# Performance work log

Measured on AMD Instinct MI355X. Metric: run time of the kernel, lower is better.

## Reference

```python
import jax, jax.numpy as jnp
import numpy as np
from jax import lax

NSAMPLE = 1024
SEM_NUM = 20


def weighted_fps(xyz, w, nsample):
    # xyz: [B,N,3], w: [B,N] -> idx [B,nsample] int32
    # Iterative weighted furthest point sampling: start at index 0, keep the
    # min squared distance to the selected set, pick argmax(min_dist * weight).
    B, N, _ = xyz.shape
    barange = jnp.arange(B)

    def step(carry, _):
        min_d, last = carry                      # [B,N], [B]
        lp = xyz[barange, last]                  # [B,3] last selected points
        d = jnp.sum((xyz - lp[:, None, :]) ** 2, axis=-1)  # [B,N]
        min_d = jnp.minimum(min_d, d)
        nxt = jnp.argmax(min_d * w, axis=1).astype(jnp.int32)
        return (min_d, nxt), nxt

    init = (jnp.full((B, N), 1e10, xyz.dtype), jnp.zeros((B,), jnp.int32))
    _, rest = lax.scan(step, init, None, length=nsample - 1)   # [nsample-1, B]
    idx = jnp.concatenate([jnp.zeros((1, B), jnp.int32), rest], axis=0)
    return idx.T                                               # [B, nsample]


def setup_inputs() -> dict:
    key = jax.random.key(0)
    k1, k2, k3 = jax.random.split(key, 3)
    B, N, C = 16, 16384, 128
    xyz = jax.random.normal(k1, (B, N, 3), dtype=jnp.float32)
    seg_feature = jax.random.normal(k2, (B, C, N), dtype=jnp.float32)
    seg_label = jax.random.randint(k3, (B, N), 0, SEM_NUM, dtype=jnp.int32)
    return {"xyz": xyz, "seg_feature": seg_feature, "seg_label": seg_label}


def reference(xyz, seg_feature, seg_label):
    # class frequency weights: count[b,c] = #points of class c in cloud b
    counts = jnp.sum(jax.nn.one_hot(seg_label, SEM_NUM, dtype=jnp.float32), axis=1)  # [B,SEM]
    seg_weights = jnp.take_along_axis(counts, seg_label, axis=1)                     # [B,N]
    idx = weighted_fps(lax.stop_gradient(xyz), seg_weights, NSAMPLE)                 # [B,S]
    sampled_xyz = jnp.take_along_axis(xyz, idx[:, :, None], axis=1)                  # [B,S,3]
    sample_seg_feature = jnp.take_along_axis(seg_feature, idx[:, None, :], axis=2)   # [B,C,S]
    sample_seg_label = jnp.take_along_axis(seg_label, idx, axis=1)                   # [B,S]
    return sampled_xyz, sample_seg_feature, sample_seg_label
```

## Files before the change

kernel.cpp:

```cpp
#include <hip/hip_runtime.h>


#define FPS_B   16
#define FPS_N   16384
#define FPS_C   128
#define FPS_S   1024
#define FPS_SEM 20
#define FPS_T   1024
#define FPS_PPT 16

__global__ __launch_bounds__(FPS_T)
__attribute__((amdgpu_waves_per_eu(4, 4)))
void wfps_kernel(
    const float* __restrict__ xyz,
    const int*   __restrict__ label,
    int*         __restrict__ idx_out)
{
  const int b = blockIdx.x;
  const int t = threadIdx.x;

  __shared__ int counts[FPS_SEM];
  __shared__ unsigned long long wmax[FPS_S];

  if (t < FPS_SEM) counts[t] = 0;
  wmax[t] = 0ull;
  __syncthreads();

  const int* lab = label + (long long)b * FPS_N;
  int mylab[FPS_PPT];
#pragma unroll
  for (int k = 0; k < FPS_PPT; ++k) {
    mylab[k] = lab[t + k * FPS_T];
    atomicAdd(&counts[mylab[k]], 1);
  }
  __syncthreads();

  const float* xb = xyz + (long long)b * FPS_N * 3;
  float px[FPS_PPT], py[FPS_PPT], pz[FPS_PPT], w[FPS_PPT], mind[FPS_PPT];
#pragma unroll
  for (int k = 0; k < FPS_PPT; ++k) {
    int n = t + k * FPS_T;
    px[k] = xb[n * 3 + 0];
    py[k] = xb[n * 3 + 1];
    pz[k] = xb[n * 3 + 2];
    w[k] = (float)counts[mylab[k]];
    mind[k] = 1e10f;
    asm("" : "+v"(px[k]), "+v"(py[k]), "+v"(pz[k]), "+v"(w[k]));
  }

  if (t == 0) idx_out[(long long)b * FPS_S] = 0;
  float lx = xb[0], ly = xb[1], lz = xb[2];

  for (int s = 1; s < FPS_S; ++s) {
    float bs = -1.0f;
    int bk = 0;
#pragma unroll
    for (int k = 0; k < FPS_PPT; ++k) {
      float dx = __fsub_rn(px[k], lx);
      float dy = __fsub_rn(py[k], ly);
      float dz = __fsub_rn(pz[k], lz);
      float d  = __fadd_rn(__fadd_rn(__fmul_rn(dx, dx), __fmul_rn(dy, dy)),
                           __fmul_rn(dz, dz));
      float m = fminf(mind[k], d);
      mind[k] = m;
      float sc = __fmul_rn(m, w[k]);
      bool g = sc > bs;
      bs = g ? sc : bs;
      bk = g ? k : bk;
    }
    unsigned n = (unsigned)t + ((unsigned)bk << 10);
    unsigned long long best =
        ((unsigned long long)__float_as_uint(bs) << 32) |
        (unsigned long long)(~n);

#pragma unroll
    for (int off = 32; off > 0; off >>= 1) {
      unsigned long long o = __shfl_xor(best, off, 64);
      best = (o > best) ? o : best;
    }
    if ((t & 63) == 0) atomicMax(&wmax[s], best);
    __syncthreads();
    best = wmax[s];

    int cur = (int)(~(unsigned)best);
    cur = __builtin_amdgcn_readfirstlane(cur);

    if (t == 0) idx_out[(long long)b * FPS_S + s] = cur;

    const float* q = xb + 3 * cur;
    lx = q[0]; ly = q[1]; lz = q[2];
  }
}

__global__ void gather_kernel(
    const float* __restrict__ xyz,
    const float* __restrict__ feat,
    const int*   __restrict__ label,
    const int*   __restrict__ idx,
    float*       __restrict__ out)
{
  const long long FEAT = (long long)FPS_B * FPS_C * FPS_S;
  const int XYZN = FPS_B * FPS_S * 3;
  const int LABN = FPS_B * FPS_S;
  long long i = (long long)blockIdx.x * blockDim.x + threadIdx.x;

  if (i < FEAT) {
    int s = (int)(i & (FPS_S - 1));
    int c = (int)((i >> 10) & (FPS_C - 1));
    int b = (int)(i >> 17);
    int n = idx[b * FPS_S + s];
    out[XYZN + i] = feat[((long long)(b * FPS_C + c)) * FPS_N + n];
  } else if (i < FEAT + XYZN) {
    int j = (int)(i - FEAT);
    int d = j % 3;
    int sb = j / 3;
    int s = sb & (FPS_S - 1);
    int b = sb >> 10;
    int n = idx[b * FPS_S + s];
    out[j] = xyz[((long long)b * FPS_N + n) * 3 + d];
  } else if (i < FEAT + XYZN + LABN) {
    int j = (int)(i - FEAT - XYZN);
    int s = j & (FPS_S - 1);
    int b = j >> 10;
    int n = idx[b * FPS_S + s];
    out[FEAT + XYZN + j] = (float)label[b * FPS_N + n];
  }
}

extern "C" void kernel_launch(void* const* d_in, const int* in_sizes, int n_in,
                              void* d_out, int out_size, void* d_ws, size_t ws_size,
                              hipStream_t stream) {
  const float* xyz   = (const float*)d_in[0];
  const float* feat  = (const float*)d_in[1];
  const int*   label = (const int*)d_in[2];
  float* out = (float*)d_out;
  int*   idx = (int*)d_ws;

  wfps_kernel<<<FPS_B, FPS_T, 0, stream>>>(xyz, label, idx);

  const long long total = (long long)FPS_B * FPS_C * FPS_S
                        + (long long)FPS_B * FPS_S * 3
                        + (long long)FPS_B * FPS_S;
  gather_kernel<<<(int)((total + 255) / 256), 256, 0, stream>>>(
      xyz, feat, label, idx, out);
}
```

Baseline: 1.892 ms.

## Split each batch's FPS across four workgroups with global-memory argmax exchange

Each point cloud's weighted FPS is spread over four workgroups instead of one, so 64 CUs work instead of 16 and each thread holds 4 points rather than 16. Every iteration, each workgroup publishes its local best to a per-step slot in global memory and spins until the other three slots are filled, then takes the max. A zeroing kernel clears the slots beforehand, and the old single-block kernel remains as a fallback when the workspace is too small. This relies on all 64 blocks being resident at once and adds a cross-CU round trip through global memory on every step.

```diff
diff --git a/kernel.cpp b/kernel.cpp
--- a/kernel.cpp
+++ b/kernel.cpp
@@ -6,56 +6,63 @@
 #define FPS_C   128
 #define FPS_S   1024
 #define FPS_SEM 20
-#define FPS_T   1024
-#define FPS_PPT 16
-
-__global__ __launch_bounds__(FPS_T)
-__attribute__((amdgpu_waves_per_eu(4, 4)))
-void wfps_kernel(
+#define FPS_QB  4
+#define FPS_MT  1024
+#define FPS_MP  4
+
+typedef unsigned long long ull;
+
+__global__ void zero_slots(ull* part) {
+  int i = blockIdx.x * blockDim.x + threadIdx.x;
+  part[i] = 0ull;
+}
+
+__global__ __launch_bounds__(FPS_MT) void wfps_multi(
     const float* __restrict__ xyz,
     const int*   __restrict__ label,
-    int*         __restrict__ idx_out)
+    int*         __restrict__ idx_out,
+    ull*         __restrict__ part)
 {
-  const int b = blockIdx.x;
+  const int b = blockIdx.x & 15;
+  const int q = blockIdx.x >> 4;
   const int t = threadIdx.x;
 
   __shared__ int counts[FPS_SEM];
-  __shared__ unsigned long long wmax[FPS_S];
+  __shared__ ull wmax[FPS_S];
 
   if (t < FPS_SEM) counts[t] = 0;
   wmax[t] = 0ull;
   __syncthreads();
 
-  const int* lab = label + (long long)b * FPS_N;
-  int mylab[FPS_PPT];
-#pragma unroll
-  for (int k = 0; k < FPS_PPT; ++k) {
-    mylab[k] = lab[t + k * FPS_T];
-    atomicAdd(&counts[mylab[k]], 1);
-  }
-  __syncthreads();
-
-  const float* xb = xyz + (long long)b * FPS_N * 3;
-  float px[FPS_PPT], py[FPS_PPT], pz[FPS_PPT], w[FPS_PPT], mind[FPS_PPT];
-#pragma unroll
-  for (int k = 0; k < FPS_PPT; ++k) {
-    int n = t + k * FPS_T;
+  const int* lab = label + b * FPS_N;
+#pragma unroll
+  for (int j = 0; j < 16; ++j)
+    atomicAdd(&counts[lab[t + j * FPS_MT]], 1);
+  __syncthreads();
+
+  const float* xb = xyz + b * FPS_N * 3;
+  float px[FPS_MP], py[FPS_MP], pz[FPS_MP], w[FPS_MP], mind[FPS_MP];
+#pragma unroll
+  for (int k = 0; k < FPS_MP; ++k) {
+    int n = q * 4096 + k * 1024 + t;
     px[k] = xb[n * 3 + 0];
     py[k] = xb[n * 3 + 1];
     pz[k] = xb[n * 3 + 2];
-    w[k] = (float)counts[mylab[k]];
+    w[k] = (float)counts[lab[n]];
     mind[k] = 1e10f;
     asm("" : "+v"(px[k]), "+v"(py[k]), "+v"(pz[k]), "+v"(w[k]));
   }
 
-  if (t == 0) idx_out[(long long)b * FPS_S] = 0;
+  if (q == 0 && t == 0) idx_out[b * FPS_S] = 0;
   float lx = xb[0], ly = xb[1], lz = xb[2];
+
+  ull* pb = part + b * (FPS_QB * FPS_S);
 
   for (int s = 1; s < FPS_S; ++s) {
     float bs = -1.0f;
     int bk = 0;
 #pragma unroll
-    for (int k = 0; k < FPS_PPT; ++k) {
+    for (int k = 0; k < FPS_MP; ++k) {
       float dx = __fsub_rn(px[k], lx);
       float dy = __fsub_rn(py[k], ly);
       float dz = __fsub_rn(pz[k], lz);
@@ -68,14 +75,114 @@
       bs = g ? sc : bs;
       bk = g ? k : bk;
     }
+    unsigned n = (unsigned)t + ((unsigned)bk << 10) + ((unsigned)q << 12);
+    ull best = ((ull)__float_as_uint(bs) << 32) | (ull)(~n);
+
+#pragma unroll
+    for (int off = 32; off > 0; off >>= 1) {
+      ull o = __shfl_xor(best, off, 64);
+      best = (o > best) ? o : best;
+    }
+    if ((t & 63) == 0) atomicMax(&wmax[s], best);
+    __syncthreads();
+
+    if (t == 0) {
+      ull loc = wmax[s];
+      __hip_atomic_store(&pb[q * FPS_S + s], loc,
+                         __ATOMIC_RELAXED, __HIP_MEMORY_SCOPE_AGENT);
+      const int q1 = (q + 1) & 3, q2 = (q + 2) & 3, q3 = (q + 3) & 3;
+      ull v1, v2, v3;
+      do {
+        v1 = __hip_atomic_load(&pb[q1 * FPS_S + s],
+                               __ATOMIC_RELAXED, __HIP_MEMORY_SCOPE_AGENT);
+        v2 = __hip_atomic_load(&pb[q2 * FPS_S + s],
+                               __ATOMIC_RELAXED, __HIP_MEMORY_SCOPE_AGENT);
+        v3 = __hip_atomic_load(&pb[q3 * FPS_S + s],
+                               __ATOMIC_RELAXED, __HIP_MEMORY_SCOPE_AGENT);
+      } while (!(v1 && v2 && v3));
+      ull m = loc;
+      m = (v1 > m) ? v1 : m;
+      m = (v2 > m) ? v2 : m;
+      m = (v3 > m) ? v3 : m;
+      wmax[s] = m;
+    }
+    __syncthreads();
+
+    ull g = wmax[s];
+    int cur = (int)(~(unsigned)g);
+    cur = __builtin_amdgcn_readfirstlane(cur);
+
+    if (q == 0 && t == 0) idx_out[b * FPS_S + s] = cur;
+
+    const float* qq = xb + 3 * cur;
+    lx = qq[0]; ly = qq[1]; lz = qq[2];
+  }
+}
+
+__global__ __launch_bounds__(1024)
+__attribute__((amdgpu_waves_per_eu(4, 4)))
+void wfps_single(
+    const float* __restrict__ xyz,
+    const int*   __restrict__ label,
+    int*         __restrict__ idx_out)
+{
+  const int b = blockIdx.x;
+  const int t = threadIdx.x;
+
+  __shared__ int counts[FPS_SEM];
+  __shared__ ull wmax[FPS_S];
+
+  if (t < FPS_SEM) counts[t] = 0;
+  wmax[t] = 0ull;
+  __syncthreads();
+
+  const int* lab = label + b * FPS_N;
+  int mylab[16];
+#pragma unroll
+  for (int k = 0; k < 16; ++k) {
+    mylab[k] = lab[t + k * 1024];
+    atomicAdd(&counts[mylab[k]], 1);
+  }
+  __syncthreads();
+
+  const float* xb = xyz + b * FPS_N * 3;
+  float px[16], py[16], pz[16], w[16], mind[16];
+#pragma unroll
+  for (int k = 0; k < 16; ++k) {
+    int n = t + k * 1024;
+    px[k] = xb[n * 3 + 0];
+    py[k] = xb[n * 3 + 1];
+    pz[k] = xb[n * 3 + 2];
+    w[k] = (float)counts[mylab[k]];
+    mind[k] = 1e10f;
+    asm("" : "+v"(px[k]), "+v"(py[k]), "+v"(pz[k]), "+v"(w[k]));
+  }
+
+  if (t == 0) idx_out[b * FPS_S] = 0;
+  float lx = xb[0], ly = xb[1], lz = xb[2];
+
+  for (int s = 1; s < FPS_S; ++s) {
+    float bs = -1.0f;
+    int bk = 0;
+#pragma unroll
+    for (int k = 0; k < 16; ++k) {
+      float dx = __fsub_rn(px[k], lx);
+      float dy = __fsub_rn(py[k], ly);
+      float dz = __fsub_rn(pz[k], lz);
+      float d  = __fadd_rn(__fadd_rn(__fmul_rn(dx, dx), __fmul_rn(dy, dy)),
+                           __fmul_rn(dz, dz));
+      float m = fminf(mind[k], d);
+      mind[k] = m;
+      float sc = __fmul_rn(m, w[k]);
+      bool g = sc > bs;
+      bs = g ? sc : bs;
+      bk = g ? k : bk;
+    }
     unsigned n = (unsigned)t + ((unsigned)bk << 10);
-    unsigned long long best =
-        ((unsigned long long)__float_as_uint(bs) << 32) |
-        (unsigned long long)(~n);
-
+    ull best = ((ull)__float_as_uint(bs) << 32) | (ull)(~n);
 #pragma unroll
     for (int off = 32; off > 0; off >>= 1) {
-      unsigned long long o = __shfl_xor(best, off, 64);
+      ull o = __shfl_xor(best, off, 64);
       best = (o > best) ? o : best;
     }
     if ((t & 63) == 0) atomicMax(&wmax[s], best);
@@ -84,11 +191,9 @@
 
     int cur = (int)(~(unsigned)best);
     cur = __builtin_amdgcn_readfirstlane(cur);
-
-    if (t == 0) idx_out[(long long)b * FPS_S + s] = cur;
-
-    const float* q = xb + 3 * cur;
-    lx = q[0]; ly = q[1]; lz = q[2];
+    if (t == 0) idx_out[b * FPS_S + s] = cur;
+    const float* qq = xb + 3 * cur;
+    lx = qq[0]; ly = qq[1]; lz = qq[2];
   }
 }
 
@@ -135,8 +240,16 @@
   const int*   label = (const int*)d_in[2];
   float* out = (float*)d_out;
   int*   idx = (int*)d_ws;
-
-  wfps_kernel<<<FPS_B, FPS_T, 0, stream>>>(xyz, label, idx);
+  ull*   part = (ull*)((char*)d_ws + 65536);
+
+  const size_t need = 65536 + (size_t)FPS_B * FPS_QB * FPS_S * 8;
+
+  if (ws_size >= need) {
+    zero_slots<<<64, 1024, 0, stream>>>(part);
+    wfps_multi<<<FPS_B * FPS_QB, FPS_MT, 0, stream>>>(xyz, label, idx, part);
+  } else {
+    wfps_single<<<FPS_B, 1024, 0, stream>>>(xyz, label, idx);
+  }
 
   const long long total = (long long)FPS_B * FPS_C * FPS_S
                         + (long long)FPS_B * FPS_S * 3
```

Result: faster. 1.854 ms, median of 2 (-2.1%).

## Use DPP wave reductions and share winner coordinates through LDS in FPS loop

Applied to the files above, without the earlier changes.

Replaces the shuffle-based wave argmax with DPP row operations followed by two cross-row shuffles. Each wave's winning lane writes its packed best value and the winner's coordinates into a double-buffered LDS slot. This removes the LDS atomicMax and the dependent global load of the selected point after the barrier. After the single barrier, every wave reduces the 16 per-wave candidates with DPP and reads the coordinates from LDS, which shortens the serial critical path of each iteration. Double buffering by step parity avoids needing a second barrier.

```diff
diff --git a/kernel.cpp b/kernel.cpp
--- a/kernel.cpp
+++ b/kernel.cpp
@@ -9,6 +9,25 @@
 #define FPS_T   1024
 #define FPS_PPT 16
 
+typedef unsigned long long ull;
+
+template <int CTRL>
+__device__ __forceinline__ ull dpp_max64(ull v) {
+  unsigned lo = (unsigned)v, hi = (unsigned)(v >> 32);
+  unsigned plo = __builtin_amdgcn_update_dpp(lo, lo, CTRL, 0xF, 0xF, true);
+  unsigned phi = __builtin_amdgcn_update_dpp(hi, hi, CTRL, 0xF, 0xF, true);
+  ull o = ((ull)phi << 32) | plo;
+  return o > v ? o : v;
+}
+
+__device__ __forceinline__ ull dpp_max16(ull v) {
+  v = dpp_max64<0xB1>(v);
+  v = dpp_max64<0x4E>(v);
+  v = dpp_max64<0x141>(v);
+  v = dpp_max64<0x140>(v);
+  return v;
+}
+
 __global__ __launch_bounds__(FPS_T)
 __attribute__((amdgpu_waves_per_eu(4, 4)))
 void wfps_kernel(
@@ -18,15 +37,17 @@
 {
   const int b = blockIdx.x;
   const int t = threadIdx.x;
+  const int wave = t >> 6;
+  const int lane = t & 63;
 
   __shared__ int counts[FPS_SEM];
-  __shared__ unsigned long long wmax[FPS_S];
+  __shared__ ull wbest[2][16];
+  __shared__ unsigned wcoord[2][16][4];
 
   if (t < FPS_SEM) counts[t] = 0;
-  wmax[t] = 0ull;
   __syncthreads();
 
-  const int* lab = label + (long long)b * FPS_N;
+  const int* lab = label + b * FPS_N;
   int mylab[FPS_PPT];
 #pragma unroll
   for (int k = 0; k < FPS_PPT; ++k) {
@@ -35,7 +56,7 @@
   }
   __syncthreads();
 
-  const float* xb = xyz + (long long)b * FPS_N * 3;
+  const float* xb = xyz + b * FPS_N * 3;
   float px[FPS_PPT], py[FPS_PPT], pz[FPS_PPT], w[FPS_PPT], mind[FPS_PPT];
 #pragma unroll
   for (int k = 0; k < FPS_PPT; ++k) {
@@ -48,7 +69,7 @@
     asm("" : "+v"(px[k]), "+v"(py[k]), "+v"(pz[k]), "+v"(w[k]));
   }
 
-  if (t == 0) idx_out[(long long)b * FPS_S] = 0;
+  if (t == 0) idx_out[b * FPS_S] = 0;
   float lx = xb[0], ly = xb[1], lz = xb[2];
 
   for (int s = 1; s < FPS_S; ++s) {
@@ -69,26 +90,35 @@
       bk = g ? k : bk;
     }
     unsigned n = (unsigned)t + ((unsigned)bk << 10);
-    unsigned long long best =
-        ((unsigned long long)__float_as_uint(bs) << 32) |
-        (unsigned long long)(~n);
+    ull best = ((ull)__float_as_uint(bs) << 32) | (ull)(~n);
 
+    best = dpp_max16(best);
+    { ull o = __shfl_xor(best, 16, 64); best = (o > best) ? o : best;
+      o = __shfl_xor(best, 32, 64);     best = (o > best) ? o : best; }
+
+    int wn = (int)(~(unsigned)best);
+    if (lane == (wn & 63)) {
+      float sx = px[0], sy = py[0], sz = pz[0];
 #pragma unroll
-    for (int off = 32; off > 0; off >>= 1) {
-      unsigned long long o = __shfl_xor(best, off, 64);
-      best = (o > best) ? o : best;
+      for (int k = 1; k < FPS_PPT; ++k)
+        if (bk == k) { sx = px[k]; sy = py[k]; sz = pz[k]; }
+      wbest[s & 1][wave] = best;
+      wcoord[s & 1][wave][0] = __float_as_uint(sx);
+      wcoord[s & 1][wave][1] = __float_as_uint(sy);
+      wcoord[s & 1][wave][2] = __float_as_uint(sz);
     }
-    if ((t & 63) == 0) atomicMax(&wmax[s], best);
     __syncthreads();
-    best = wmax[s];
 
-    int cur = (int)(~(unsigned)best);
-    cur = __builtin_amdgcn_readfirstlane(cur);
+    ull v = wbest[s & 1][lane & 15];
+    v = dpp_max16(v);
+    int cur = (int)(~(unsigned)v);
+    int r = (cur >> 6) & 15;
 
-    if (t == 0) idx_out[(long long)b * FPS_S + s] = cur;
+    lx = __uint_as_float(wcoord[s & 1][r][0]);
+    ly = __uint_as_float(wcoord[s & 1][r][1]);
+    lz = __uint_as_float(wcoord[s & 1][r][2]);
 
-    const float* q = xb + 3 * cur;
-    lx = q[0]; ly = q[1]; lz = q[2];
+    if (t == 0) idx_out[b * FPS_S + s] = cur;
   }
 }
 
```

Result: slower. 2.422 ms (+28.0%).
